# Optimization experiments

Measured on AMD Instinct MI355X. Metric: run time of the kernel, lower is better.

The kernel has to match this reference:

```python
import jax, jax.numpy as jnp
import numpy as np

H = W = 512; CELL = 8; P = 16; GX = GY = 64; NGH = GX // 2
SHIFTS = ((0, 0), (1, 0), (0, 1), (1, 1))
EPS = 1e-8
TWO_PI = 2.0 * np.pi

def _diff_round(x):
    return x - jnp.sin(x * TWO_PI) / TWO_PI

def _harder_diff_round(x):
    return _diff_round(_diff_round(x))

def _patches(pad_arr, sx, sy):
    # pad_arr: (H+2*CELL, W+2*CELL, C) -> (NGH*NGH, P, P, C) overlapping supervoxel patches
    x0 = sx * CELL + CELL - (P - CELL) // 2
    y0 = sy * CELL + CELL - (P - CELL) // 2
    s = pad_arr[x0:x0 + NGH * P, y0:y0 + NGH * P]
    c = s.shape[-1]
    return s.reshape(NGH, P, NGH, P, c).transpose(0, 2, 1, 3, 4).reshape(NGH * NGH, P, P, c)

def _conv_trio(x, w, b):
    y = jax.lax.conv_general_dilated(x, w, (1, 1), 'SAME', dimension_numbers=('NHWC', 'HWIO', 'NHWC'))
    return jax.nn.relu(y + b)

def _mlp(x, w0, b0, w1, b1, w2, b2, w3, b3):
    # mlp_features=[5,5,5] with relu, final linear projection to latent_size=10
    x = jax.nn.relu(x @ w0 + b0)
    x = jax.nn.relu(x @ w1 + b1)
    x = jax.nn.relu(x @ w2 + b2)
    return x @ w3 + b3

def _forward(curr_image, curr_label, masks, conv1_w, conv1_b, conv2_w, conv2_b, dense1_w, dense1_b,
             we0, be0, we1, be1, we2, be2, we3, be3, wn0, bn0, wn1, bn1, wn2, bn2, wn3, bn3,
             wout, bout, senders, receivers):
    ids = jnp.arange(GX * GY, dtype=masks.dtype).reshape(GX, GY)
    img, lab, msk = curr_image[0], curr_label[0], masks[0]
    pad_img = jnp.pad(img, ((CELL, CELL), (CELL, CELL), (0, 0)))
    pad_lab = jnp.pad(lab, ((CELL, CELL), (CELL, CELL), (0, 0)))
    pad_msk = jnp.pad(msk[..., None], ((CELL, CELL), (CELL, CELL), (0, 0)), constant_values=-1.0)
    toks, lsv = [], []
    for sx, sy in SHIFTS:  # fixed 4 shift groups (structural, not data loop)
        cid = ids[sx::2, sy::2].reshape(-1)                                    # (F,)
        filt = (_patches(pad_msk, sx, sy)[..., 0] == cid[:, None, None]).astype(img.dtype)  # (F,P,P)
        toks.append(_patches(pad_img, sx, sy) * filt[..., None])              # masked image patches
        lp = _patches(pad_lab, sx, sy)[..., 0]
        summ = jnp.sum(filt, axis=(1, 2))
        lsv.append(_harder_diff_round(jnp.sum(lp * filt, axis=(1, 2)) / (summ + EPS)))
    tokens = jnp.concatenate(toks, axis=0)      # (N, P, P, 1), N = GX*GY
    label_svs = jnp.concatenate(lsv, axis=0)    # (N,)
    x = _conv_trio(tokens, conv1_w, conv1_b)
    x = _conv_trio(x, conv2_w, conv2_b)
    nodes = jax.nn.relu(x.reshape(x.shape[0], -1) @ dense1_w + dense1_b)      # (N, 6)
    n = nodes.shape[0]; e = senders.shape[0]
    ones_e = jnp.ones((e, 1), nodes.dtype)      # broadcast global context [[1]]
    edge_feat = _mlp(jnp.concatenate([nodes[senders], nodes[receivers], ones_e], -1),
                     we0, be0, we1, be1, we2, be2, we3, be3)                   # (E, 10)
    agg = jax.ops.segment_sum(edge_feat, receivers, num_segments=n)            # (N, 10)
    ones_n = jnp.ones((n, 1), nodes.dtype)
    new_nodes = _mlp(jnp.concatenate([nodes, agg, ones_n], -1),
                     wn0, bn0, wn1, bn1, wn2, bn2, wn3, bn3)                   # (N, 10)
    logits = new_nodes @ wout + bout                                           # (N, 2)
    labels2 = jnp.stack([1.0 - label_svs, label_svs], axis=-1)
    return -jnp.sum(labels2 * jax.nn.log_softmax(logits, axis=-1), axis=-1)    # (N,)

def setup_inputs():
    key = jax.random.key(0)
    ks = jax.random.split(key, 32)
    def w(i, shape):
        fan = int(np.prod(shape[:-1]))
        return jax.random.normal(ks[i], shape, jnp.float32) / np.sqrt(fan)
    curr_image = jax.random.normal(ks[0], (1, H, W, 1), jnp.float32)
    curr_label = (jax.random.uniform(ks[1], (1, H, W, 1)) > 0.5).astype(jnp.float32)
    # masks: per-pixel supervoxel id = id of containing 8x8 grid cell
    ids = np.arange(GX * GY, dtype=np.float32).reshape(GX, GY)
    masks = jnp.asarray(np.repeat(np.repeat(ids, CELL, 0), CELL, 1))[None]  # (1, H, W)
    # node index consistent with group-concatenation order of tokens
    node_id = np.zeros((GX, GY), dtype=np.int32)
    for g, (sx, sy) in enumerate(SHIFTS):
        node_id[sx::2, sy::2] = g * NGH * NGH + np.arange(NGH * NGH, dtype=np.int32).reshape(NGH, NGH)
    a = node_id[:, :-1].ravel(); b = node_id[:, 1:].ravel()
    c = node_id[:-1, :].ravel(); d = node_id[1:, :].ravel()
    senders = jnp.asarray(np.concatenate([a, b, c, d]))     # (16128,)
    receivers = jnp.asarray(np.concatenate([b, a, d, c]))
    return dict(curr_image=curr_image, curr_label=curr_label, masks=masks,
                conv1_w=w(2, (3, 3, 1, 40)), conv1_b=jnp.zeros((40,), jnp.float32),
                conv2_w=w(3, (3, 3, 40, 40)), conv2_b=jnp.zeros((40,), jnp.float32),
                dense1_w=w(4, (P * P * 40, 6)), dense1_b=jnp.zeros((6,), jnp.float32),
                we0=w(5, (13, 5)), be0=jnp.zeros((5,), jnp.float32),
                we1=w(6, (5, 5)), be1=jnp.zeros((5,), jnp.float32),
                we2=w(7, (5, 5)), be2=jnp.zeros((5,), jnp.float32),
                we3=w(8, (5, 10)), be3=jnp.zeros((10,), jnp.float32),
                wn0=w(9, (17, 5)), bn0=jnp.zeros((5,), jnp.float32),
                wn1=w(10, (5, 5)), bn1=jnp.zeros((5,), jnp.float32),
                wn2=w(11, (5, 5)), bn2=jnp.zeros((5,), jnp.float32),
                wn3=w(12, (5, 10)), bn3=jnp.zeros((10,), jnp.float32),
                wout=w(13, (10, 2)), bout=jnp.zeros((2,), jnp.float32),
                senders=senders, receivers=receivers)

def reference(curr_image, curr_label, masks, conv1_w, conv1_b, conv2_w, conv2_b, dense1_w, dense1_b,
              we0, be0, we1, be1, we2, be2, we3, be3, wn0, bn0, wn1, bn1, wn2, bn2, wn3, bn3,
              wout, bout, senders, receivers):
    return _forward(curr_image, curr_label, masks, conv1_w, conv1_b, conv2_w, conv2_b, dense1_w, dense1_b,
                    we0, be0, we1, be1, we2, be2, we3, be3, wn0, bn0, wn1, bn1, wn2, bn2, wn3, bn3,
                    wout, bout, senders, receivers)
```

## Files before the change

kernel.cpp:

```cpp
#include <hip/hip_runtime.h>
#include <math.h>


typedef __attribute__((ext_vector_type(8))) short short8;
typedef __attribute__((ext_vector_type(4))) float f32x4;

#define ZROW  324
#define NWTB  (12 * 4 * 48 * 8)
#define ND1W  (256 * 48 * 8)

static __device__ __forceinline__ unsigned short f2bf(float x) {
    unsigned int u = __float_as_uint(x);
    u += 0x7FFF + ((u >> 16) & 1);
    return (unsigned short)(u >> 16);
}

static __device__ __forceinline__ float diff_round(float x) {
    const float TP = 6.2831853071795864769f;
    return x - sinf(x * TP) / TP;
}

template<int IN, int OUT>
static __device__ __forceinline__ void mlp_layer(const float* in,
                                                 const float* __restrict__ w,
                                                 const float* __restrict__ b,
                                                 float* out, bool do_relu) {
#pragma unroll
    for (int j = 0; j < OUT; ++j) {
        float a = b[j];
#pragma unroll
        for (int i = 0; i < IN; ++i) a = fmaf(in[i], w[i * OUT + j], a);
        out[j] = do_relu ? fmaxf(a, 0.f) : a;
    }
}

__global__ __launch_bounds__(256) void k_prep(const float* __restrict__ w2,
                                              const float* __restrict__ d1w,
                                              unsigned short* __restrict__ wTbG,
                                              unsigned short* __restrict__ d1wb) {
    const int i = blockIdx.x * 256 + threadIdx.x;
    if (i < NWTB) {
        const int j    = i & 7;
        const int co   = (i >> 3) % 48;
        const int qg   = (i >> 3) / 48;
        const int quad = qg & 3;
        const int grp  = qg >> 2;
        float val = 0.f;
        if (grp < 9) {
            if (co < 40) val = w2[(grp * 40 + quad * 8 + j) * 40 + co];
        } else {
            const int tap = (grp - 9) * 4 + quad;
            if (tap < 9 && co < 40) val = w2[(tap * 40 + 32 + j) * 40 + co];
        }
        wTbG[i] = f2bf(val);
    } else if (i < NWTB + ND1W) {
        const int jj = i - NWTB;
        const int k  = jj & 7;
        const int co = (jj >> 3) % 48;
        const int px = (jj >> 3) / 48;
        d1wb[jj] = f2bf((co < 40 && k < 6) ? d1w[(px * 40 + co) * 6 + k] : 0.f);
    }
}

__global__ __launch_bounds__(512, 4) void k_patch(
    const float* __restrict__ img, const float* __restrict__ lab,
    const float* __restrict__ msk,
    const float* __restrict__ w1, const float* __restrict__ b1,
    const unsigned short* __restrict__ wTbG,
    const float* __restrict__ b2,
    const unsigned short* __restrict__ d1wb, const float* __restrict__ d1b,
    float* __restrict__ nodes, float* __restrict__ lsv)
{
    __shared__ __align__(16) unsigned short x1[325 * 40];
    __shared__ __align__(16) unsigned short Bs[NWTB];
    __shared__ float p[256];
    __shared__ float red[4][2];
    __shared__ float wsum[8][6];

    const int n = blockIdx.x;
    const int t = threadIdx.x;
    const int g = n >> 10, cell = n & 1023;
    const int gi = cell >> 5, gj = cell & 31;
    const int sx = g & 1, sy = g >> 1;
    const int gx = sx + 2 * gi, gy = sy + 2 * gj;
    const int px0 = gx * 8 - 4, py0 = gy * 8 - 4;
    const float cid = (float)(gx * 64 + gy);

    const int ph = t >> 8, pix = t & 255;
    const int u = pix >> 4, v = pix & 15;
    const int lane = t & 63, wv = t >> 6;
    const int lane15 = t & 15, quad = (t >> 4) & 3;

    float m = -1.f, iv = 0.f, lv = 0.f;
    if (ph == 0) {
        const int r = px0 + u, c = py0 + v;
        if (r >= 0 && r < 512 && c >= 0 && c < 512) {
            m  = msk[r * 512 + c];
            iv = img[r * 512 + c];
            lv = lab[r * 512 + c];
        }
    }

    {
        const uint4* src = (const uint4*)wTbG;
        uint4* dst = (uint4*)Bs;
        for (int i = t; i < NWTB / 8; i += 512) dst[i] = src[i];
    }

    {
        unsigned int* x1w = (unsigned int*)x1;
        for (int i = t; i < 69 * 20; i += 512) {
            const int cellI = i / 20, d = i - cellI * 20;
            int cr;
            if      (cellI < 18) cr = cellI;
            else if (cellI < 36) cr = cellI + 288;
            else if (cellI < 52) cr = (cellI - 35) * 18;
            else if (cellI < 68) cr = (cellI - 51) * 18 + 17;
            else                 cr = ZROW;
            x1w[cr * 20 + d] = 0u;
        }
    }

    const float f = (m == cid) ? 1.f : 0.f;
    if (ph == 0) {
        p[pix] = iv * f;
        float sf = f, slf = lv * f;
        for (int off = 32; off; off >>= 1) {
            sf  += __shfl_down(sf,  off);
            slf += __shfl_down(slf, off);
        }
        if (lane == 0) { red[wv][0] = sf; red[wv][1] = slf; }
    }
    __syncthreads();

    if (t == 0) {
        const float SF = red[0][0] + red[1][0] + red[2][0] + red[3][0];
        const float SL = red[0][1] + red[1][1] + red[2][1] + red[3][1];
        lsv[n] = diff_round(diff_round(SL / (SF + 1e-8f)));
    }

    {
        float nbv[9];
#pragma unroll
        for (int ky = 0; ky < 3; ++ky)
#pragma unroll
            for (int kx = 0; kx < 3; ++kx) {
                const int uy = u + ky - 1, vx = v + kx - 1;
                const bool ok = (uy >= 0) && (uy < 16) && (vx >= 0) && (vx < 16);
                nbv[ky * 3 + kx] = ok ? p[uy * 16 + vx] : 0.f;
            }
        float a1[20];
#pragma unroll
        for (int cc = 0; cc < 20; ++cc) a1[cc] = b1[ph * 20 + cc];
#pragma unroll
        for (int k = 0; k < 9; ++k) {
            const float xv = nbv[k];
#pragma unroll
            for (int cc = 0; cc < 20; ++cc)
                a1[cc] = fmaf(xv, w1[k * 40 + ph * 20 + cc], a1[cc]);
        }
        const int row = (u + 1) * 18 + (v + 1);
        unsigned int* x1w = (unsigned int*)x1;
#pragma unroll
        for (int cg = 0; cg < 10; ++cg) {
            const unsigned int lo = f2bf(fmaxf(a1[2 * cg], 0.f));
            const unsigned int hi = f2bf(fmaxf(a1[2 * cg + 1], 0.f));
            x1w[row * 20 + ph * 10 + cg] = lo | (hi << 16);
        }
    }
    __syncthreads();

    float bias[3];
#pragma unroll
    for (int nt = 0; nt < 3; ++nt) {
        const int co = nt * 16 + lane15;
        bias[nt] = (co < 40) ? b2[co] : 0.f;
    }
    f32x4 acc[2][3];
#pragma unroll
    for (int mt = 0; mt < 2; ++mt)
#pragma unroll
        for (int nt = 0; nt < 3; ++nt) {
            acc[mt][nt][0] = bias[nt]; acc[mt][nt][1] = bias[nt];
            acc[mt][nt][2] = bias[nt]; acc[mt][nt][3] = bias[nt];
        }

#pragma unroll
    for (int tap = 0; tap < 9; ++tap) {
        const int ky = tap / 3, kx = tap % 3;
        short8 bf[3];
#pragma unroll
        for (int nt = 0; nt < 3; ++nt)
            bf[nt] = *(const short8*)(Bs + ((tap * 4 + quad) * 48 + nt * 16 + lane15) * 8);
#pragma unroll
        for (int mt = 0; mt < 2; ++mt) {
            const int arow = (wv * 2 + mt + ky) * 18 + (lane15 + kx);
            const short8 a0 = *(const short8*)(x1 + arow * 40 + quad * 8);
#pragma unroll
            for (int nt = 0; nt < 3; ++nt)
                acc[mt][nt] = __builtin_amdgcn_mfma_f32_16x16x32_bf16(
                    a0, bf[nt], acc[mt][nt], 0, 0, 0);
        }
    }
#pragma unroll
    for (int s = 0; s < 3; ++s) {
        short8 bt[3];
#pragma unroll
        for (int nt = 0; nt < 3; ++nt)
            bt[nt] = *(const short8*)(Bs + (((9 + s) * 4 + quad) * 48 + nt * 16 + lane15) * 8);
        const int tapq = s * 4 + quad;
        const int kyq  = (tapq * 11) >> 5;
        const int kxq  = tapq - 3 * kyq;
#pragma unroll
        for (int mt = 0; mt < 2; ++mt) {
            const int arowq = (wv * 2 + mt + kyq) * 18 + (lane15 + kxq);
            const int offs  = (tapq < 9) ? (arowq * 40 + 32) : (ZROW * 40);
            const short8 at = *(const short8*)(x1 + offs);
#pragma unroll
            for (int nt = 0; nt < 3; ++nt)
                acc[mt][nt] = __builtin_amdgcn_mfma_f32_16x16x32_bf16(
                    at, bt[nt], acc[mt][nt], 0, 0, 0);
        }
    }

    float a6[6] = {0.f, 0.f, 0.f, 0.f, 0.f, 0.f};
#pragma unroll
    for (int mt = 0; mt < 2; ++mt)
#pragma unroll
        for (int nt = 0; nt < 3; ++nt) {
            const int co = nt * 16 + lane15;
#pragma unroll
            for (int reg = 0; reg < 4; ++reg) {
                const int pixel = (wv * 2 + mt) * 16 + quad * 4 + reg;
                const uint4 wq = *(const uint4*)(d1wb + ((pixel * 48 + co) << 3));
                const float a = fmaxf(acc[mt][nt][reg], 0.f);
                a6[0] = fmaf(a, __uint_as_float(wq.x << 16),          a6[0]);
                a6[1] = fmaf(a, __uint_as_float(wq.x & 0xFFFF0000u),  a6[1]);
                a6[2] = fmaf(a, __uint_as_float(wq.y << 16),          a6[2]);
                a6[3] = fmaf(a, __uint_as_float(wq.y & 0xFFFF0000u),  a6[3]);
                a6[4] = fmaf(a, __uint_as_float(wq.z << 16),          a6[4]);
                a6[5] = fmaf(a, __uint_as_float(wq.z & 0xFFFF0000u),  a6[5]);
            }
        }
    for (int off = 32; off; off >>= 1) {
#pragma unroll
        for (int k = 0; k < 6; ++k) a6[k] += __shfl_down(a6[k], off);
    }
    if (lane == 0) {
#pragma unroll
        for (int k = 0; k < 6; ++k) wsum[wv][k] = a6[k];
    }
    __syncthreads();
    if (t < 6) {
        float s = d1b[t];
#pragma unroll
        for (int w = 0; w < 8; ++w) s += wsum[w][t];
        nodes[n * 6 + t] = fmaxf(s, 0.f);
    }
}


#define OWE0 0
#define OBE0 65
#define OWE1 70
#define OBE1 95
#define OWE2 100
#define OBE2 125
#define OWE3 130
#define OBE3 180
#define OWN0 190
#define OBN0 275
#define OWN1 280
#define OBN1 305
#define OWN2 310
#define OBN2 335
#define OWN3 340
#define OBN3 390
#define OWOUT 400
#define OBOUT 420
#define NWPOOL 422

__global__ __launch_bounds__(64) void k_node(
    const float* __restrict__ nodes, const float* __restrict__ lsv,
    const float* __restrict__ we0, const float* __restrict__ be0,
    const float* __restrict__ we1, const float* __restrict__ be1,
    const float* __restrict__ we2, const float* __restrict__ be2,
    const float* __restrict__ we3, const float* __restrict__ be3,
    const float* __restrict__ wn0, const float* __restrict__ bn0,
    const float* __restrict__ wn1, const float* __restrict__ bn1,
    const float* __restrict__ wn2, const float* __restrict__ bn2,
    const float* __restrict__ wn3, const float* __restrict__ bn3,
    const float* __restrict__ wout, const float* __restrict__ bout,
    float* __restrict__ out, int N)
{
    __shared__ float L[NWPOOL];
    const int t = threadIdx.x;

    {
        const float* srcs[18] = {we0, be0, we1, be1, we2, be2, we3, be3,
                                 wn0, bn0, wn1, bn1, wn2, bn2, wn3, bn3,
                                 wout, bout};
        const int lens[18] = {65, 5, 25, 5, 25, 5, 50, 10,
                              85, 5, 25, 5, 25, 5, 50, 10, 20, 2};
        int off = 0;
        for (int a = 0; a < 18; ++a) {
            for (int i = t; i < lens[a]; i += 64) L[off + i] = srcs[a][i];
            off += lens[a];
        }
    }
    __syncthreads();

    const int n = blockIdx.x * 16 + (t >> 2);
    const int d = t & 3;
    const bool nvalid = n < N;

    const int g = n >> 10, cell = n & 1023;
    const int gi = cell >> 5, gj = cell & 31;
    const int gx = (g & 1) + 2 * gi, gy = (g >> 1) + 2 * gj;

    float self6[6];
#pragma unroll
    for (int i = 0; i < 6; ++i) self6[i] = nvalid ? nodes[n * 6 + i] : 0.f;

    const int DX[4] = {0, 0, -1, 1};
    const int DY[4] = {-1, 1, 0, 0};
    const int x = gx + DX[d], y = gy + DY[d];
    const bool ev = nvalid && x >= 0 && x < 64 && y >= 0 && y < 64;

    float o10[10];
#pragma unroll
    for (int j = 0; j < 10; ++j) o10[j] = 0.f;
    if (ev) {
        const int mid = ((x & 1) + 2 * (y & 1)) * 1024 + (x >> 1) * 32 + (y >> 1);
        float in13[13];
#pragma unroll
        for (int i = 0; i < 6; ++i) in13[i] = nodes[mid * 6 + i];
#pragma unroll
        for (int i = 0; i < 6; ++i) in13[6 + i] = self6[i];
        in13[12] = 1.f;
        float h0[5], h1[5], h2[5];
        mlp_layer<13, 5>(in13, L + OWE0, L + OBE0, h0, true);
        mlp_layer<5, 5>(h0, L + OWE1, L + OBE1, h1, true);
        mlp_layer<5, 5>(h1, L + OWE2, L + OBE2, h2, true);
        mlp_layer<5, 10>(h2, L + OWE3, L + OBE3, o10, false);
    }

    float agg[10];
#pragma unroll
    for (int j = 0; j < 10; ++j) {
        float v = o10[j];
        v += __shfl_xor(v, 1);
        v += __shfl_xor(v, 2);
        agg[j] = v;
    }

    float in17[17];
#pragma unroll
    for (int i = 0; i < 6; ++i)  in17[i]     = self6[i];
#pragma unroll
    for (int i = 0; i < 10; ++i) in17[6 + i] = agg[i];
    in17[16] = 1.f;
    float h0[5], h1[5], h2[5], o[10];
    mlp_layer<17, 5>(in17, L + OWN0, L + OBN0, h0, true);
    mlp_layer<5, 5>(h0, L + OWN1, L + OBN1, h1, true);
    mlp_layer<5, 5>(h1, L + OWN2, L + OBN2, h2, true);
    mlp_layer<5, 10>(h2, L + OWN3, L + OBN3, o, false);

    float l0 = L[OBOUT + 0], l1 = L[OBOUT + 1];
#pragma unroll
    for (int i = 0; i < 10; ++i) {
        l0 = fmaf(o[i], L[OWOUT + i * 2 + 0], l0);
        l1 = fmaf(o[i], L[OWOUT + i * 2 + 1], l1);
    }
    if (d == 0 && nvalid) {
        const float mx  = fmaxf(l0, l1);
        const float e0  = expf(l0 - mx), e1 = expf(l1 - mx);
        const float lse = mx + logf(e0 + e1);
        const float sv  = lsv[n];
        out[n] = -((1.f - sv) * (l0 - lse) + sv * (l1 - lse));
    }
}

extern "C" void kernel_launch(void* const* d_in, const int* in_sizes, int n_in,
                              void* d_out, int out_size, void* d_ws, size_t ws_size,
                              hipStream_t stream) {
    (void)n_in; (void)ws_size; (void)in_sizes;
    const float* img = (const float*)d_in[0];
    const float* lab = (const float*)d_in[1];
    const float* msk = (const float*)d_in[2];
    const float* w1  = (const float*)d_in[3];
    const float* b1  = (const float*)d_in[4];
    const float* w2  = (const float*)d_in[5];
    const float* b2  = (const float*)d_in[6];
    const float* d1w = (const float*)d_in[7];
    const float* d1b = (const float*)d_in[8];
    const float* we0 = (const float*)d_in[9],  *be0 = (const float*)d_in[10];
    const float* we1 = (const float*)d_in[11], *be1 = (const float*)d_in[12];
    const float* we2 = (const float*)d_in[13], *be2 = (const float*)d_in[14];
    const float* we3 = (const float*)d_in[15], *be3 = (const float*)d_in[16];
    const float* wn0 = (const float*)d_in[17], *bn0 = (const float*)d_in[18];
    const float* wn1 = (const float*)d_in[19], *bn1 = (const float*)d_in[20];
    const float* wn2 = (const float*)d_in[21], *bn2 = (const float*)d_in[22];
    const float* wn3 = (const float*)d_in[23], *bn3 = (const float*)d_in[24];
    const float* wout = (const float*)d_in[25], *bout = (const float*)d_in[26];
    const int N = out_size;

    char* base = (char*)d_ws;
    float* nodes = (float*)base;
    float* lsvb  = (float*)(base + (size_t)N * 6 * 4);
    unsigned short* wTbG = (unsigned short*)(base + (size_t)N * 7 * 4);
    unsigned short* d1wb = wTbG + NWTB;
    float* out   = (float*)d_out;

    const int prep_n = NWTB + ND1W;
    k_prep<<<(prep_n + 255) / 256, 256, 0, stream>>>(w2, d1w, wTbG, d1wb);
    k_patch<<<N, 512, 0, stream>>>(img, lab, msk, w1, b1, wTbG, b2,
                                   d1wb, d1b, nodes, lsvb);
    k_node<<<(N + 15) / 16, 64, 0, stream>>>(nodes, lsvb,
                                             we0, be0, we1, be1, we2, be2,
                                             we3, be3,
                                             wn0, bn0, wn1, bn1, wn2, bn2,
                                             wn3, bn3, wout, bout, out, N);
}
```

Baseline: 219.6 us.

## Compact conv2 weight and dense1 layouts to shrink LDS and raise occupancy

Conv2 bf16 weights are repacked into a 40-channel layout for the nine main taps, so the shared-memory copy drops the padding channels and the tail channel-group weights are read straight from global memory. The dense1 weights are packed densely as 6 values per channel instead of padded 8-wide rows, and lanes for padded output channels read a dummy address. Launch bounds are raised from 4 to 6 blocks per CU so the smaller LDS footprint can be used for more resident blocks. The costs are extra global loads for the tail taps, unaligned 32-bit weight loads instead of 128-bit ones, and tighter register limits.

```diff
diff --git a/kernel.cpp b/kernel.cpp
--- a/kernel.cpp
+++ b/kernel.cpp
@@ -7,7 +7,8 @@
 
 #define ZROW  324
 #define NWTB  (12 * 4 * 48 * 8)
-#define ND1W  (256 * 48 * 8)
+#define NW40  (9 * 4 * 40 * 8)
+#define ND1W  (256 * 40 * 6)
 
 static __device__ __forceinline__ unsigned short f2bf(float x) {
     unsigned int u = __float_as_uint(x);
@@ -37,6 +38,7 @@
 __global__ __launch_bounds__(256) void k_prep(const float* __restrict__ w2,
                                               const float* __restrict__ d1w,
                                               unsigned short* __restrict__ wTbG,
+                                              unsigned short* __restrict__ wT40,
                                               unsigned short* __restrict__ d1wb) {
     const int i = blockIdx.x * 256 + threadIdx.x;
     if (i < NWTB) {
@@ -53,26 +55,35 @@
             if (tap < 9 && co < 40) val = w2[(tap * 40 + 32 + j) * 40 + co];
         }
         wTbG[i] = f2bf(val);
-    } else if (i < NWTB + ND1W) {
-        const int jj = i - NWTB;
-        const int k  = jj & 7;
-        const int co = (jj >> 3) % 48;
-        const int px = (jj >> 3) / 48;
-        d1wb[jj] = f2bf((co < 40 && k < 6) ? d1w[(px * 40 + co) * 6 + k] : 0.f);
-    }
-}
-
-__global__ __launch_bounds__(512, 4) void k_patch(
+    } else if (i < NWTB + NW40) {
+        const int i2   = i - NWTB;
+        const int j    = i2 & 7;
+        const int co   = (i2 >> 3) % 40;
+        const int tq   = (i2 >> 3) / 40;
+        const int quad = tq & 3;
+        const int tap  = tq >> 2;
+        wT40[i2] = f2bf(w2[(tap * 40 + quad * 8 + j) * 40 + co]);
+    } else if (i < NWTB + NW40 + ND1W) {
+        const int i3 = i - NWTB - NW40;
+        const int k  = i3 % 6;
+        const int co = (i3 / 6) % 40;
+        const int px = (i3 / 6) / 40;
+        d1wb[i3] = f2bf(d1w[(px * 40 + co) * 6 + k]);
+    }
+}
+
+__global__ __launch_bounds__(512, 6) void k_patch(
     const float* __restrict__ img, const float* __restrict__ lab,
     const float* __restrict__ msk,
     const float* __restrict__ w1, const float* __restrict__ b1,
     const unsigned short* __restrict__ wTbG,
+    const unsigned short* __restrict__ wT40,
     const float* __restrict__ b2,
     const unsigned short* __restrict__ d1wb, const float* __restrict__ d1b,
     float* __restrict__ nodes, float* __restrict__ lsv)
 {
     __shared__ __align__(16) unsigned short x1[325 * 40];
-    __shared__ __align__(16) unsigned short Bs[NWTB];
+    __shared__ __align__(16) unsigned short Bs[NW40];
     __shared__ float p[256];
     __shared__ float red[4][2];
     __shared__ float wsum[8][6];
@@ -90,6 +101,7 @@
     const int u = pix >> 4, v = pix & 15;
     const int lane = t & 63, wv = t >> 6;
     const int lane15 = t & 15, quad = (t >> 4) & 3;
+    const bool hi8 = lane15 >= 8;
 
     float m = -1.f, iv = 0.f, lv = 0.f;
     if (ph == 0) {
@@ -102,9 +114,9 @@
     }
 
     {
-        const uint4* src = (const uint4*)wTbG;
+        const uint4* src = (const uint4*)wT40;
         uint4* dst = (uint4*)Bs;
-        for (int i = t; i < NWTB / 8; i += 512) dst[i] = src[i];
+        for (int i = t; i < NW40 / 8; i += 512) dst[i] = src[i];
     }
 
     {
@@ -185,13 +197,17 @@
             acc[mt][nt][2] = bias[nt]; acc[mt][nt][3] = bias[nt];
         }
 
+    const unsigned short* zrow16 = x1 + ZROW * 40;
+
 #pragma unroll
     for (int tap = 0; tap < 9; ++tap) {
         const int ky = tap / 3, kx = tap % 3;
+        const int bb = (tap * 4 + quad) * 40;
         short8 bf[3];
-#pragma unroll
-        for (int nt = 0; nt < 3; ++nt)
-            bf[nt] = *(const short8*)(Bs + ((tap * 4 + quad) * 48 + nt * 16 + lane15) * 8);
+        bf[0] = *(const short8*)(Bs + (bb + lane15) * 8);
+        bf[1] = *(const short8*)(Bs + (bb + 16 + lane15) * 8);
+        bf[2] = hi8 ? *(const short8*)zrow16
+                    : *(const short8*)(Bs + (bb + 32 + lane15) * 8);
 #pragma unroll
         for (int mt = 0; mt < 2; ++mt) {
             const int arow = (wv * 2 + mt + ky) * 18 + (lane15 + kx);
@@ -207,7 +223,7 @@
         short8 bt[3];
 #pragma unroll
         for (int nt = 0; nt < 3; ++nt)
-            bt[nt] = *(const short8*)(Bs + (((9 + s) * 4 + quad) * 48 + nt * 16 + lane15) * 8);
+            bt[nt] = *(const short8*)(wTbG + (((9 + s) * 4 + quad) * 48 + nt * 16 + lane15) * 8);
         const int tapq = s * 4 + quad;
         const int kyq  = (tapq * 11) >> 5;
         const int kxq  = tapq - 3 * kyq;
@@ -223,23 +239,28 @@
         }
     }
 
+    const unsigned int* d1u = (const unsigned int*)d1wb;
     float a6[6] = {0.f, 0.f, 0.f, 0.f, 0.f, 0.f};
 #pragma unroll
     for (int mt = 0; mt < 2; ++mt)
 #pragma unroll
         for (int nt = 0; nt < 3; ++nt) {
             const int co = nt * 16 + lane15;
+            const bool dead = (nt == 2) && hi8;
 #pragma unroll
             for (int reg = 0; reg < 4; ++reg) {
                 const int pixel = (wv * 2 + mt) * 16 + quad * 4 + reg;
-                const uint4 wq = *(const uint4*)(d1wb + ((pixel * 48 + co) << 3));
+                const int dwb = dead ? 0 : (pixel * 40 + co) * 3;
+                const unsigned int w0 = d1u[dwb];
+                const unsigned int w1v = d1u[dwb + 1];
+                const unsigned int w2v = d1u[dwb + 2];
                 const float a = fmaxf(acc[mt][nt][reg], 0.f);
-                a6[0] = fmaf(a, __uint_as_float(wq.x << 16),          a6[0]);
-                a6[1] = fmaf(a, __uint_as_float(wq.x & 0xFFFF0000u),  a6[1]);
-                a6[2] = fmaf(a, __uint_as_float(wq.y << 16),          a6[2]);
-                a6[3] = fmaf(a, __uint_as_float(wq.y & 0xFFFF0000u),  a6[3]);
-                a6[4] = fmaf(a, __uint_as_float(wq.z << 16),          a6[4]);
-                a6[5] = fmaf(a, __uint_as_float(wq.z & 0xFFFF0000u),  a6[5]);
+                a6[0] = fmaf(a, __uint_as_float(w0 << 16),           a6[0]);
+                a6[1] = fmaf(a, __uint_as_float(w0 & 0xFFFF0000u),   a6[1]);
+                a6[2] = fmaf(a, __uint_as_float(w1v << 16),          a6[2]);
+                a6[3] = fmaf(a, __uint_as_float(w1v & 0xFFFF0000u),  a6[3]);
+                a6[4] = fmaf(a, __uint_as_float(w2v << 16),          a6[4]);
+                a6[5] = fmaf(a, __uint_as_float(w2v & 0xFFFF0000u),  a6[5]);
             }
         }
     for (int off = 32; off; off >>= 1) {
@@ -409,12 +430,13 @@
     float* nodes = (float*)base;
     float* lsvb  = (float*)(base + (size_t)N * 6 * 4);
     unsigned short* wTbG = (unsigned short*)(base + (size_t)N * 7 * 4);
-    unsigned short* d1wb = wTbG + NWTB;
+    unsigned short* wT40 = wTbG + NWTB;
+    unsigned short* d1wb = wT40 + NW40;
     float* out   = (float*)d_out;
 
-    const int prep_n = NWTB + ND1W;
-    k_prep<<<(prep_n + 255) / 256, 256, 0, stream>>>(w2, d1w, wTbG, d1wb);
-    k_patch<<<N, 512, 0, stream>>>(img, lab, msk, w1, b1, wTbG, b2,
+    const int prep_n = NWTB + NW40 + ND1W;
+    k_prep<<<(prep_n + 255) / 256, 256, 0, stream>>>(w2, d1w, wTbG, wT40, d1wb);
+    k_patch<<<N, 512, 0, stream>>>(img, lab, msk, w1, b1, wTbG, wT40, b2,
                                    d1wb, d1b, nodes, lsvb);
     k_node<<<(N + 15) / 16, 64, 0, stream>>>(nodes, lsvb,
                                              we0, be0, we1, be1, we2, be2,
```

Result: slower. 327.9 us (+49.3%).
